# Optimization experiments

Measured on AMD Instinct MI355X. Metric: run time of the kernel, lower is better.

The kernel has to match this reference:

```python
import jax, jax.numpy as jnp
import numpy as np

TOKENS, HIDDEN = 2048, 1024
N_EXPERTS, INTER, TOPK = 8, 2816, 2
RENORMALIZE = True


def setup_inputs() -> dict:
    key = jax.random.key(0)
    k1, k2, k3, k4 = jax.random.split(key, 4)
    x = jax.random.normal(k1, (TOKENS, HIDDEN), dtype=jnp.float32)
    gating_output = jax.random.normal(k2, (TOKENS, N_EXPERTS), dtype=jnp.float32)
    # stacked gate_proj+up_proj per expert: [E, 2*I, H]
    w1 = jax.random.normal(k3, (N_EXPERTS, 2 * INTER, HIDDEN), dtype=jnp.float32) * 0.02
    # down_proj per expert: [E, H, I]
    w2 = jax.random.normal(k4, (N_EXPERTS, HIDDEN, INTER), dtype=jnp.float32) * 0.02
    return {"x": x, "gating_output": gating_output, "w1": w1, "w2": w2}


def _moe(x, gating_output, w1, w2):
    # fused_topk: softmax over router logits, then top-k, then renormalize
    probs = jax.nn.softmax(gating_output, axis=-1)              # [T, E]
    topk_w, topk_ids = jax.lax.top_k(probs, TOPK)                # [T, K]
    if RENORMALIZE:
        topk_w = topk_w / jnp.sum(topk_w, axis=-1, keepdims=True)
    # fused_experts: gate/up proj -> SiLU(gate)*up -> down proj, per expert
    h = jnp.einsum('th,eih->tei', x, w1)                         # [T, E, 2I]
    gate, up = h[..., :INTER], h[..., INTER:]
    act = jax.nn.silu(gate) * up                                 # [T, E, I]
    out_e = jnp.einsum('tei,ehi->teh', act, w2)                  # [T, E, H]
    # combine: gather selected experts and weight them
    sel = jnp.take_along_axis(out_e, topk_ids[:, :, None], axis=1)  # [T, K, H]
    return jnp.sum(sel * topk_w[:, :, None].astype(sel.dtype), axis=1)  # [T, H]


def reference(x, gating_output, w1, w2):
    return _moe(x, gating_output, w1, w2)
```

## Files before the change

kernel.cpp:

```cpp
#include <hip/hip_runtime.h>
#include <hip/hip_bf16.h>

#define TOKENS 2048
#define HIDDEN 1024
#define NEXP   8
#define INTER  2816
#define N1     5632
#define ROWCAP 6144
#define MT     24
#define NT1    44
#define NT2    8
#define SPLITK 2

typedef __attribute__((ext_vector_type(8))) short short8;
typedef __attribute__((ext_vector_type(4))) float f32x4;

typedef unsigned int __attribute__((address_space(1))) as1_uint;
typedef unsigned int __attribute__((address_space(3))) as3_uint;

__device__ __forceinline__ void gload16(const void* g, void* l) {
  __builtin_amdgcn_global_load_lds((const as1_uint*)g, (as3_uint*)l, 16, 0, 0);
}

__device__ __forceinline__ unsigned short f2bf(float f) {
  unsigned u = __float_as_uint(f);
  u += 0x7fff + ((u >> 16) & 1);
  return (unsigned short)(u >> 16);
}
__device__ __forceinline__ float bf2f(unsigned short h) {
  return __uint_as_float(((unsigned)h) << 16);
}
__device__ __forceinline__ unsigned short bfs(float x) {
  __hip_bfloat16 h = __float2bfloat16(x);
  return *reinterpret_cast<unsigned short*>(&h);
}
__device__ __forceinline__ short8 pack8(f32x4 lo, f32x4 hi) {
  short8 o;
  o[0] = (short)bfs(lo[0]); o[1] = (short)bfs(lo[1]); o[2] = (short)bfs(lo[2]); o[3] = (short)bfs(lo[3]);
  o[4] = (short)bfs(hi[0]); o[5] = (short)bfs(hi[1]); o[6] = (short)bfs(hi[2]); o[7] = (short)bfs(hi[3]);
  return o;
}

__global__ void k_routing(const float* __restrict__ gate, int* __restrict__ ctrl,
                          int* __restrict__ tkid, float* __restrict__ tkw) {
  int t = blockIdx.x * blockDim.x + threadIdx.x;
  if (t >= TOKENS) return;
  float l[8];
#pragma unroll
  for (int i = 0; i < 8; i++) l[i] = gate[t * 8 + i];
  int i0 = 0; float m0 = l[0];
#pragma unroll
  for (int i = 1; i < 8; i++) if (l[i] > m0) { m0 = l[i]; i0 = i; }
  int i1 = -1; float m1 = -3.4e38f;
#pragma unroll
  for (int i = 0; i < 8; i++) if (i != i0 && l[i] > m1) { m1 = l[i]; i1 = i; }
  float e  = __expf(m1 - m0);
  float w0 = 1.f / (1.f + e);
  float w1 = e / (1.f + e);
  tkid[2 * t] = i0; tkid[2 * t + 1] = i1;
  tkw[2 * t] = w0;  tkw[2 * t + 1] = w1;
  atomicAdd(&ctrl[i0], 1);
  atomicAdd(&ctrl[i1], 1);
}

__global__ void k_base(int* ctrl) {
  if (threadIdx.x == 0) {
    int a = 0;
    for (int e = 0; e < 8; e++) { ctrl[16 + e] = a; a += ((ctrl[e] + 255) >> 8) << 8; }
  }
}

__global__ void k_fill(int* __restrict__ ctrl, const int* __restrict__ tkid,
                       int* __restrict__ rtok, int* __restrict__ trow) {
  int t = blockIdx.x * blockDim.x + threadIdx.x;
  if (t >= TOKENS) return;
#pragma unroll
  for (int k = 0; k < 2; k++) {
    int e = tkid[2 * t + k];
    int pos = atomicAdd(&ctrl[8 + e], 1);
    int row = ctrl[16 + e] + pos;
    rtok[row] = t;
    trow[2 * t + k] = row;
  }
}

__global__ void k_gather(const float* __restrict__ x, const int* __restrict__ ctrl,
                         const int* __restrict__ rtok, unsigned short* __restrict__ Abf) {
  int row = blockIdx.x;
  int e = -1, local = 0;
  for (int i = 0; i < 8; i++) {
    int b = ctrl[16 + i], p = ((ctrl[i] + 255) >> 8) << 8;
    if (row >= b && row < b + p) { e = i; local = row - b; break; }
  }
  if (e < 0) return;
  int tid = threadIdx.x;
  unsigned short* dst = Abf + (size_t)row * HIDDEN;
  if (local < ctrl[e]) {
    int t = rtok[row];
    float4 v = ((const float4*)(x + (size_t)t * HIDDEN))[tid];
    ushort4 o; o.x = f2bf(v.x); o.y = f2bf(v.y); o.z = f2bf(v.z); o.w = f2bf(v.w);
    ((ushort4*)dst)[tid] = o;
  } else {
    ushort4 z; z.x = 0; z.y = 0; z.z = 0; z.w = 0;
    ((ushort4*)dst)[tid] = z;
  }
}

__device__ __forceinline__ int tile_lookup(const int* ctrl, int mt, int* ml) {
  int a0 = 0;
  for (int i = 0; i < 8; i++) {
    int pt = (ctrl[i] + 255) >> 8;
    if (mt < a0 + pt) { *ml = mt - a0; return i; }
    a0 += pt;
  }
  return -1;
}

__global__ __launch_bounds__(512, 2) void k_gemm1(const float* __restrict__ w1,
    const unsigned short* __restrict__ Abf, unsigned short* __restrict__ act,
    const int* __restrict__ ctrl) {
  union __align__(16) LdsU {
    struct { unsigned char A0[32768]; unsigned char Bf0[32768];
             unsigned char A1[32768]; unsigned char Bf1[32768]; } st;
    unsigned short hb[256 * 132];
  };
  __shared__ LdsU lds;
  int bid = blockIdx.x;
  int wg = (bid & 7) * (NT1 * MT / 8) + (bid >> 3);
  int nt = wg / MT, mt = wg % MT;
  int ml; int e = tile_lookup(ctrl, mt, &ml);
  if (e < 0) return;
  int tid = threadIdx.x, lane = tid & 63, wid = tid >> 6, wr = wid >> 1, wc = wid & 1;
  int rbase = ctrl[16 + e] + ml * 256;
  const unsigned char* Ab = (const unsigned char*)(Abf + (size_t)rbase * HIDDEN);
  const unsigned char* Bw = (const unsigned char*)(w1 + (size_t)e * N1 * HIDDEN);
  int l3 = lane >> 3, l4 = lane >> 4, l15 = lane & 15;
  int swzA = ((lane & 7) ^ l3) << 4;

  unsigned aoff[4], boff[4];
#pragma unroll
  for (int i = 0; i < 4; i++) {
    int g = wid * 4 + i;
    aoff[i] = (unsigned)(g * 8 + l3) * (HIDDEN * 2) + swzA;
  }
#pragma unroll
  for (int i = 0; i < 4; i++) {
    int r = (wid * 4 + i) * 4 + l4;
    int grow = (r < 64) ? nt * 64 + r : INTER + nt * 64 + (r - 64);
    boff[i] = (unsigned)grow * (HIDDEN * 4) + ((l15 ^ (r & 15)) << 4);
  }

  f32x4 acc[4][4];
  f32x4 zero = {0.f, 0.f, 0.f, 0.f};
#pragma unroll
  for (int i = 0; i < 4; i++)
#pragma unroll
    for (int j = 0; j < 4; j++) acc[i][j] = zero;

#define STG1(kk, Ad, Bd) do {                                                        \
  _Pragma("unroll") for (int i = 0; i < 4; i++)                                      \
    gload16(Ab + (size_t)aoff[i] + (kk) * 128, &(Ad)[(wid * 4 + i) * 1024]);         \
  _Pragma("unroll") for (int i = 0; i < 4; i++)                                      \
    gload16(Bw + (size_t)boff[i] + (kk) * 256, &(Bd)[(wid * 4 + i) * 1024]);         \
} while (0)

#define CMP1(Ad, Bd) do {                                                            \
  _Pragma("unroll") for (int ks = 0; ks < 2; ++ks) {                                 \
    short8 a[4], b[4];                                                               \
    _Pragma("unroll") for (int mi = 0; mi < 4; mi++) {                               \
      int row = wr * 64 + mi * 16 + l15;                                             \
      int koff = ks * 64 + (l4 << 4);                                                \
      a[mi] = *(const short8*)&(Ad)[row * 128 + (koff ^ ((row & 7) << 4))];          \
    }                                                                                \
    _Pragma("unroll") for (int ni = 0; ni < 4; ni++) {                               \
      int r = wc * 64 + ni * 16 + l15;                                               \
      int c = ks * 8 + l4 * 2;                                                       \
      f32x4 lo = *(const f32x4*)&(Bd)[r * 256 + ((c ^ (r & 15)) << 4)];              \
      f32x4 hi = *(const f32x4*)&(Bd)[r * 256 + (((c + 1) ^ (r & 15)) << 4)];        \
      b[ni] = pack8(lo, hi);                                                         \
    }                                                                                \
    _Pragma("unroll") for (int mi = 0; mi < 4; mi++)                                 \
      _Pragma("unroll") for (int ni = 0; ni < 4; ni++)                               \
        acc[mi][ni] = __builtin_amdgcn_mfma_f32_16x16x32_bf16(a[mi], b[ni], acc[mi][ni], 0, 0, 0); \
  }                                                                                  \
} while (0)

  const int NS = HIDDEN / 64;
  STG1(0, lds.st.A0, lds.st.Bf0);
  __syncthreads();
  for (int s = 0; s < NS; s += 2) {
    STG1(s + 1, lds.st.A1, lds.st.Bf1);
    CMP1(lds.st.A0, lds.st.Bf0);
    __syncthreads();
    if (s + 2 < NS) STG1(s + 2, lds.st.A0, lds.st.Bf0);
    CMP1(lds.st.A1, lds.st.Bf1);
    __syncthreads();
  }
#undef STG1
#undef CMP1

#pragma unroll
  for (int mi = 0; mi < 4; mi++)
#pragma unroll
    for (int ni = 0; ni < 4; ni++)
#pragma unroll
      for (int r = 0; r < 4; r++) {
        int row = wr * 64 + mi * 16 + (l4 << 2) + r;
        int col = wc * 64 + ni * 16 + l15;
        lds.hb[row * 132 + col] = f2bf(acc[mi][ni][r]);
      }
  __syncthreads();
  {
    int r = tid >> 1, ch = (tid & 1) * 32;
    unsigned short* orow = act + (size_t)(rbase + r) * INTER + nt * 64 + ch;
    const unsigned short* hrow = &lds.hb[r * 132];
#pragma unroll
    for (int j = 0; j < 32; j += 4) {
      ushort4 o;
#pragma unroll
      for (int q = 0; q < 4; q++) {
        float g = bf2f(hrow[ch + j + q]);
        float u = bf2f(hrow[64 + ch + j + q]);
        float s = g / (1.f + __expf(-g));
        ((unsigned short*)&o)[q] = f2bf(s * u);
      }
      *(ushort4*)(orow + j) = o;
    }
  }
}

__global__ __launch_bounds__(512, 2) void k_gemm2(const float* __restrict__ w2,
    const unsigned short* __restrict__ act, float* __restrict__ Pb,
    const int* __restrict__ ctrl) {
  struct __align__(16) Lds2 { unsigned char A0[32768]; unsigned char Bf0[32768];
                              unsigned char A1[32768]; unsigned char Bf1[32768]; };
  __shared__ Lds2 lds;
  int bid = blockIdx.x;
  int wg = (bid & 7) * (NT2 * MT * SPLITK / 8) + (bid >> 3);
  int mt = wg % MT;
  int p = wg / MT;
  int z = p & 1, nt = p >> 1;
  int ml; int e = tile_lookup(ctrl, mt, &ml);
  if (e < 0) return;
  int tid = threadIdx.x, lane = tid & 63, wid = tid >> 6, wr = wid >> 1, wc = wid & 1;
  int rbase = ctrl[16 + e] + ml * 256;
  const int KST = (INTER / 64) / SPLITK;
  const unsigned char* Ab = (const unsigned char*)(act + (size_t)rbase * INTER) + (size_t)z * KST * 128;
  const unsigned char* Bw = (const unsigned char*)(w2 + (size_t)e * HIDDEN * INTER) + (size_t)z * KST * 256;
  int l3 = lane >> 3, l4 = lane >> 4, l15 = lane & 15;
  int swzA = ((lane & 7) ^ l3) << 4;

  unsigned aoff[4], boff[4];
#pragma unroll
  for (int i = 0; i < 4; i++) {
    int g = wid * 4 + i;
    aoff[i] = (unsigned)(g * 8 + l3) * (INTER * 2) + swzA;
  }
#pragma unroll
  for (int i = 0; i < 4; i++) {
    int r = (wid * 4 + i) * 4 + l4;
    boff[i] = (unsigned)(nt * 128 + r) * (INTER * 4) + ((l15 ^ (r & 15)) << 4);
  }

  f32x4 acc[4][4];
  f32x4 zero = {0.f, 0.f, 0.f, 0.f};
#pragma unroll
  for (int i = 0; i < 4; i++)
#pragma unroll
    for (int j = 0; j < 4; j++) acc[i][j] = zero;

#define STG2(kk, Ad, Bd) do {                                                        \
  _Pragma("unroll") for (int i = 0; i < 4; i++)                                      \
    gload16(Ab + (size_t)aoff[i] + (kk) * 128, &(Ad)[(wid * 4 + i) * 1024]);         \
  _Pragma("unroll") for (int i = 0; i < 4; i++)                                      \
    gload16(Bw + (size_t)boff[i] + (kk) * 256, &(Bd)[(wid * 4 + i) * 1024]);         \
} while (0)

#define CMP2(Ad, Bd) do {                                                            \
  _Pragma("unroll") for (int ks = 0; ks < 2; ++ks) {                                 \
    short8 a[4], b[4];                                                               \
    _Pragma("unroll") for (int mi = 0; mi < 4; mi++) {                               \
      int row = wr * 64 + mi * 16 + l15;                                             \
      int koff = ks * 64 + (l4 << 4);                                                \
      a[mi] = *(const short8*)&(Ad)[row * 128 + (koff ^ ((row & 7) << 4))];          \
    }                                                                                \
    _Pragma("unroll") for (int ni = 0; ni < 4; ni++) {                               \
      int r = wc * 64 + ni * 16 + l15;                                               \
      int c = ks * 8 + l4 * 2;                                                       \
      f32x4 lo = *(const f32x4*)&(Bd)[r * 256 + ((c ^ (r & 15)) << 4)];              \
      f32x4 hi = *(const f32x4*)&(Bd)[r * 256 + (((c + 1) ^ (r & 15)) << 4)];        \
      b[ni] = pack8(lo, hi);                                                         \
    }                                                                                \
    _Pragma("unroll") for (int mi = 0; mi < 4; mi++)                                 \
      _Pragma("unroll") for (int ni = 0; ni < 4; ni++)                               \
        acc[mi][ni] = __builtin_amdgcn_mfma_f32_16x16x32_bf16(a[mi], b[ni], acc[mi][ni], 0, 0, 0); \
  }                                                                                  \
} while (0)

  STG2(0, lds.A0, lds.Bf0);
  __syncthreads();
  for (int s = 0; s < KST; s += 2) {
    STG2(s + 1, lds.A1, lds.Bf1);
    CMP2(lds.A0, lds.Bf0);
    __syncthreads();
    if (s + 2 < KST) STG2(s + 2, lds.A0, lds.Bf0);
    CMP2(lds.A1, lds.Bf1);
    __syncthreads();
  }
#undef STG2
#undef CMP2

  float* P = Pb + (size_t)z * ROWCAP * HIDDEN;
#pragma unroll
  for (int mi = 0; mi < 4; mi++)
#pragma unroll
    for (int ni = 0; ni < 4; ni++) {
      int col = nt * 128 + wc * 64 + ni * 16 + l15;
#pragma unroll
      for (int r = 0; r < 4; r++) {
        int row = rbase + wr * 64 + mi * 16 + (l4 << 2) + r;
        P[(size_t)row * HIDDEN + col] = acc[mi][ni][r];
      }
    }
}

__global__ void k_finish(const float* __restrict__ Pb,
                         const int* __restrict__ trow, const float* __restrict__ tkw,
                         float* __restrict__ out) {
  int t = blockIdx.x, c = threadIdx.x;
  const float* P0 = Pb;
  const float* P1 = Pb + (size_t)ROWCAP * HIDDEN;
  int r0 = trow[2 * t], r1 = trow[2 * t + 1];
  float w0 = tkw[2 * t], w1 = tkw[2 * t + 1];
  float4 a0 = ((const float4*)(P0 + (size_t)r0 * HIDDEN))[c];
  float4 b0 = ((const float4*)(P1 + (size_t)r0 * HIDDEN))[c];
  float4 a1 = ((const float4*)(P0 + (size_t)r1 * HIDDEN))[c];
  float4 b1 = ((const float4*)(P1 + (size_t)r1 * HIDDEN))[c];
  float4 o;
  o.x = w0 * (a0.x + b0.x) + w1 * (a1.x + b1.x);
  o.y = w0 * (a0.y + b0.y) + w1 * (a1.y + b1.y);
  o.z = w0 * (a0.z + b0.z) + w1 * (a1.z + b1.z);
  o.w = w0 * (a0.w + b0.w) + w1 * (a1.w + b1.w);
  ((float4*)(out + (size_t)t * HIDDEN))[c] = o;
}

extern "C" void kernel_launch(void* const* d_in, const int* in_sizes, int n_in,
                              void* d_out, int out_size, void* d_ws, size_t ws_size,
                              hipStream_t stream) {
  const float* x      = (const float*)d_in[0];
  const float* gating = (const float*)d_in[1];
  const float* w1     = (const float*)d_in[2];
  const float* w2     = (const float*)d_in[3];
  float* out = (float*)d_out;
  char* ws = (char*)d_ws;

  int*   ctrl = (int*)ws;
  int*   tkid = (int*)(ws + 4096);
  float* tkw  = (float*)(ws + 24576);
  int*   rtok = (int*)(ws + 45056);
  int*   trow = (int*)(ws + 73728);
  size_t off_Abf = 131072;
  size_t off_act = off_Abf + (size_t)ROWCAP * HIDDEN * 2;
  size_t off_P   = off_act + (size_t)ROWCAP * INTER * 2;
  unsigned short* Abf  = (unsigned short*)(ws + off_Abf);
  unsigned short* actb = (unsigned short*)(ws + off_act);
  float* Pb = (float*)(ws + off_P);

  hipMemsetAsync(ws, 0, 1024, stream);

  k_routing<<<TOKENS / 256, 256, 0, stream>>>(gating, ctrl, tkid, tkw);
  k_base<<<1, 64, 0, stream>>>(ctrl);
  k_fill<<<TOKENS / 256, 256, 0, stream>>>(ctrl, tkid, rtok, trow);
  k_gather<<<ROWCAP, 256, 0, stream>>>(x, ctrl, rtok, Abf);
  k_gemm1<<<NT1 * MT, 512, 0, stream>>>(w1, Abf, actb, ctrl);
  k_gemm2<<<NT2 * MT * SPLITK, 512, 0, stream>>>(w2, actb, Pb, ctrl);
  k_finish<<<TOKENS, 256, 0, stream>>>(Pb, trow, tkw, out);
}
```

Before: 277.4 us.

## Restructure GEMM mainloops with staggered A/B prefetch, manual waitcnts and MFMA priority

Replaces the two-stage __syncthreads pipeline in both expert GEMMs with a finer-grained schedule. A is prefetched one k-tile ahead and B two tiles ahead. The loop uses raw s_barrier with explicit vmcnt/lgkmcnt waits, splits each k-tile into interleaved LDS-read/MFMA phases, and raises wave priority around MFMA bursts. The aim is to hide global-to-LDS latency and LDS reads behind matrix math. It adds hand-tuned waitcnt counts that are easy to get wrong and cause races, plus extra barriers per tile.

```diff
diff --git a/kernel.cpp b/kernel.cpp
--- a/kernel.cpp
+++ b/kernel.cpp
@@ -40,6 +40,11 @@
   o[4] = (short)bfs(hi[0]); o[5] = (short)bfs(hi[1]); o[6] = (short)bfs(hi[2]); o[7] = (short)bfs(hi[3]);
   return o;
 }
+
+#define BARRIER() asm volatile("s_barrier" ::: "memory")
+#define VMW4()    asm volatile("s_waitcnt vmcnt(4)" ::: "memory")
+#define VMW0()    asm volatile("s_waitcnt vmcnt(0)" ::: "memory")
+#define LGKM0()   asm volatile("s_waitcnt lgkmcnt(0)" ::: "memory")
 
 __global__ void k_routing(const float* __restrict__ gate, int* __restrict__ ctrl,
                           int* __restrict__ tkid, float* __restrict__ tkw) {
@@ -116,12 +121,68 @@
   return -1;
 }
 
+
+#define STGA(kk, Ad, Abase) do {                                                      \
+  _Pragma("unroll") for (int i_ = 0; i_ < 4; i_++)                                    \
+    gload16((Abase) + (size_t)aoff[i_] + (size_t)(kk) * 128, &(Ad)[(wid * 4 + i_) * 1024]); \
+} while (0)
+
+#define STGB(kk, Bd, Bbase) do {                                                      \
+  _Pragma("unroll") for (int i_ = 0; i_ < 4; i_++)                                    \
+    gload16((Bbase) + (size_t)boff[i_] + (size_t)(kk) * 256, &(Bd)[(wid * 4 + i_) * 1024]); \
+} while (0)
+
+#define LDA_F(Ad, mi, ks)                                                              \
+  (*(const short8*)&(Ad)[(wr * 64 + (mi) * 16 + l15) * 128 +                           \
+     ((((ks) * 64 + (l4 << 4))) ^ ((l15 & 7) << 4))])
+
+#define LDB_F(Bd, ni, ks, dst) do {                                                    \
+  int r_ = wc * 64 + (ni) * 16 + l15;                                                  \
+  int c_ = (ks) * 8 + l4 * 2;                                                          \
+  f32x4 lo_ = *(const f32x4*)&(Bd)[r_ * 256 + ((c_ ^ (r_ & 15)) << 4)];                \
+  f32x4 hi_ = *(const f32x4*)&(Bd)[r_ * 256 + (((c_ + 1) ^ (r_ & 15)) << 4)];          \
+  dst = pack8(lo_, hi_);                                                               \
+} while (0)
+
+#define MFMA8(m0, a0_, a1_) do {                                                       \
+  __builtin_amdgcn_s_setprio(1);                                                       \
+  _Pragma("unroll") for (int ni_ = 0; ni_ < 4; ni_++)                                  \
+    acc[(m0)][ni_] = __builtin_amdgcn_mfma_f32_16x16x32_bf16(a0_, bb[ni_], acc[(m0)][ni_], 0, 0, 0); \
+  _Pragma("unroll") for (int ni_ = 0; ni_ < 4; ni_++)                                  \
+    acc[(m0)+1][ni_] = __builtin_amdgcn_mfma_f32_16x16x32_bf16(a1_, bb[ni_], acc[(m0)+1][ni_], 0, 0, 0); \
+  __builtin_amdgcn_s_setprio(0);                                                       \
+} while (0)
+
+#define KTILE(t, NTILES, CA, CB, NA, Abase, Bbase) do {                                 \
+  if ((t) + 1 < (NTILES)) STGA((t) + 1, NA, Abase);                                     \
+  { short8 a0 = LDA_F(CA, 0, 0), a1 = LDA_F(CA, 1, 0);                                  \
+    LDB_F(CB, 0, 0, bb[0]); LDB_F(CB, 1, 0, bb[1]);                                     \
+    LDB_F(CB, 2, 0, bb[2]); LDB_F(CB, 3, 0, bb[3]);                                     \
+    MFMA8(0, a0, a1); }                                                                 \
+  BARRIER();                                                                            \
+  { short8 a2 = LDA_F(CA, 2, 0), a3 = LDA_F(CA, 3, 0);                                  \
+    MFMA8(2, a2, a3); }                                                                 \
+  BARRIER();                                                                            \
+  { short8 a0 = LDA_F(CA, 0, 1), a1 = LDA_F(CA, 1, 1);                                  \
+    LDB_F(CB, 0, 1, bb[0]); LDB_F(CB, 1, 1, bb[1]);                                     \
+    LDB_F(CB, 2, 1, bb[2]); LDB_F(CB, 3, 1, bb[3]);                                     \
+    MFMA8(0, a0, a1); }                                                                 \
+  LGKM0();                                                                              \
+  BARRIER();                                                                            \
+  { short8 a2 = LDA_F(CA, 2, 1), a3 = LDA_F(CA, 3, 1);                                  \
+    if ((t) + 2 < (NTILES)) STGB((t) + 2, CB, Bbase);                                   \
+    MFMA8(2, a2, a3); }                                                                 \
+  if ((t) + 2 < (NTILES)) { VMW4(); } else { VMW0(); }                                  \
+  LGKM0();                                                                              \
+  BARRIER();                                                                            \
+} while (0)
+
 __global__ __launch_bounds__(512, 2) void k_gemm1(const float* __restrict__ w1,
     const unsigned short* __restrict__ Abf, unsigned short* __restrict__ act,
     const int* __restrict__ ctrl) {
   union __align__(16) LdsU {
-    struct { unsigned char A0[32768]; unsigned char Bf0[32768];
-             unsigned char A1[32768]; unsigned char Bf1[32768]; } st;
+    struct { unsigned char A0[32768]; unsigned char B0[32768];
+             unsigned char A1[32768]; unsigned char B1[32768]; } st;
     unsigned short hb[256 * 132];
   };
   __shared__ LdsU lds;
@@ -156,48 +217,18 @@
   for (int i = 0; i < 4; i++)
 #pragma unroll
     for (int j = 0; j < 4; j++) acc[i][j] = zero;
-
-#define STG1(kk, Ad, Bd) do {                                                        \
-  _Pragma("unroll") for (int i = 0; i < 4; i++)                                      \
-    gload16(Ab + (size_t)aoff[i] + (kk) * 128, &(Ad)[(wid * 4 + i) * 1024]);         \
-  _Pragma("unroll") for (int i = 0; i < 4; i++)                                      \
-    gload16(Bw + (size_t)boff[i] + (kk) * 256, &(Bd)[(wid * 4 + i) * 1024]);         \
-} while (0)
-
-#define CMP1(Ad, Bd) do {                                                            \
-  _Pragma("unroll") for (int ks = 0; ks < 2; ++ks) {                                 \
-    short8 a[4], b[4];                                                               \
-    _Pragma("unroll") for (int mi = 0; mi < 4; mi++) {                               \
-      int row = wr * 64 + mi * 16 + l15;                                             \
-      int koff = ks * 64 + (l4 << 4);                                                \
-      a[mi] = *(const short8*)&(Ad)[row * 128 + (koff ^ ((row & 7) << 4))];          \
-    }                                                                                \
-    _Pragma("unroll") for (int ni = 0; ni < 4; ni++) {                               \
-      int r = wc * 64 + ni * 16 + l15;                                               \
-      int c = ks * 8 + l4 * 2;                                                       \
-      f32x4 lo = *(const f32x4*)&(Bd)[r * 256 + ((c ^ (r & 15)) << 4)];              \
-      f32x4 hi = *(const f32x4*)&(Bd)[r * 256 + (((c + 1) ^ (r & 15)) << 4)];        \
-      b[ni] = pack8(lo, hi);                                                         \
-    }                                                                                \
-    _Pragma("unroll") for (int mi = 0; mi < 4; mi++)                                 \
-      _Pragma("unroll") for (int ni = 0; ni < 4; ni++)                               \
-        acc[mi][ni] = __builtin_amdgcn_mfma_f32_16x16x32_bf16(a[mi], b[ni], acc[mi][ni], 0, 0, 0); \
-  }                                                                                  \
-} while (0)
+  short8 bb[4];
 
   const int NS = HIDDEN / 64;
-  STG1(0, lds.st.A0, lds.st.Bf0);
-  __syncthreads();
-  for (int s = 0; s < NS; s += 2) {
-    STG1(s + 1, lds.st.A1, lds.st.Bf1);
-    CMP1(lds.st.A0, lds.st.Bf0);
-    __syncthreads();
-    if (s + 2 < NS) STG1(s + 2, lds.st.A0, lds.st.Bf0);
-    CMP1(lds.st.A1, lds.st.Bf1);
-    __syncthreads();
-  }
-#undef STG1
-#undef CMP1
+  STGA(0, lds.st.A0, Ab);
+  STGB(0, lds.st.B0, Bw);
+  STGB(1, lds.st.B1, Bw);
+  VMW4();
+  BARRIER();
+  for (int t = 0; t < NS; t += 2) {
+    KTILE(t,     NS, lds.st.A0, lds.st.B0, lds.st.A1, Ab, Bw);
+    KTILE(t + 1, NS, lds.st.A1, lds.st.B1, lds.st.A0, Ab, Bw);
+  }
 
 #pragma unroll
   for (int mi = 0; mi < 4; mi++)
@@ -232,8 +263,8 @@
 __global__ __launch_bounds__(512, 2) void k_gemm2(const float* __restrict__ w2,
     const unsigned short* __restrict__ act, float* __restrict__ Pb,
     const int* __restrict__ ctrl) {
-  struct __align__(16) Lds2 { unsigned char A0[32768]; unsigned char Bf0[32768];
-                              unsigned char A1[32768]; unsigned char Bf1[32768]; };
+  struct __align__(16) Lds2 { unsigned char A0[32768]; unsigned char B0[32768];
+                              unsigned char A1[32768]; unsigned char B1[32768]; };
   __shared__ Lds2 lds;
   int bid = blockIdx.x;
   int wg = (bid & 7) * (NT2 * MT * SPLITK / 8) + (bid >> 3);
@@ -268,47 +299,17 @@
   for (int i = 0; i < 4; i++)
 #pragma unroll
     for (int j = 0; j < 4; j++) acc[i][j] = zero;
-
-#define STG2(kk, Ad, Bd) do {                                                        \
-  _Pragma("unroll") for (int i = 0; i < 4; i++)                                      \
-    gload16(Ab + (size_t)aoff[i] + (kk) * 128, &(Ad)[(wid * 4 + i) * 1024]);         \
-  _Pragma("unroll") for (int i = 0; i < 4; i++)                                      \
-    gload16(Bw + (size_t)boff[i] + (kk) * 256, &(Bd)[(wid * 4 + i) * 1024]);         \
-} while (0)
-
-#define CMP2(Ad, Bd) do {                                                            \
-  _Pragma("unroll") for (int ks = 0; ks < 2; ++ks) {                                 \
-    short8 a[4], b[4];                                                               \
-    _Pragma("unroll") for (int mi = 0; mi < 4; mi++) {                               \
-      int row = wr * 64 + mi * 16 + l15;                                             \
-      int koff = ks * 64 + (l4 << 4);                                                \
-      a[mi] = *(const short8*)&(Ad)[row * 128 + (koff ^ ((row & 7) << 4))];          \
-    }                                                                                \
-    _Pragma("unroll") for (int ni = 0; ni < 4; ni++) {                               \
-      int r = wc * 64 + ni * 16 + l15;                                               \
-      int c = ks * 8 + l4 * 2;                                                       \
-      f32x4 lo = *(const f32x4*)&(Bd)[r * 256 + ((c ^ (r & 15)) << 4)];              \
-      f32x4 hi = *(const f32x4*)&(Bd)[r * 256 + (((c + 1) ^ (r & 15)) << 4)];        \
-      b[ni] = pack8(lo, hi);                                                         \
-    }                                                                                \
-    _Pragma("unroll") for (int mi = 0; mi < 4; mi++)                                 \
-      _Pragma("unroll") for (int ni = 0; ni < 4; ni++)                               \
-        acc[mi][ni] = __builtin_amdgcn_mfma_f32_16x16x32_bf16(a[mi], b[ni], acc[mi][ni], 0, 0, 0); \
-  }                                                                                  \
-} while (0)
-
-  STG2(0, lds.A0, lds.Bf0);
-  __syncthreads();
-  for (int s = 0; s < KST; s += 2) {
-    STG2(s + 1, lds.A1, lds.Bf1);
-    CMP2(lds.A0, lds.Bf0);
-    __syncthreads();
-    if (s + 2 < KST) STG2(s + 2, lds.A0, lds.Bf0);
-    CMP2(lds.A1, lds.Bf1);
-    __syncthreads();
-  }
-#undef STG2
-#undef CMP2
+  short8 bb[4];
+
+  STGA(0, lds.A0, Ab);
+  STGB(0, lds.B0, Bw);
+  STGB(1, lds.B1, Bw);
+  VMW4();
+  BARRIER();
+  for (int t = 0; t < KST; t += 2) {
+    KTILE(t,     KST, lds.A0, lds.B0, lds.A1, Ab, Bw);
+    KTILE(t + 1, KST, lds.A1, lds.B1, lds.A0, Ab, Bw);
+  }
 
   float* P = Pb + (size_t)z * ROWCAP * HIDDEN;
 #pragma unroll
```

New measurement: 257.4 us. 1.08x faster.
